# Kernel optimization log

Measured on AMD Instinct MI355X. Metric: run time of the kernel, lower is better.

Reference implementation:

```python
import jax, jax.numpy as jnp
import numpy as np

N = 2_000_000
FEAT = 128
S = 8192


def setup_inputs() -> dict:
    key = jax.random.key(0)
    k1, k2, k3, k4, k5 = jax.random.split(key, 5)
    x = jax.random.normal(k1, (N, FEAT), dtype=jnp.float32)
    subst_ids = jax.random.randint(k2, (N,), 0, S, dtype=jnp.int32)
    W1 = jax.random.normal(k3, (FEAT, 64), dtype=jnp.float32) * (1.0 / np.sqrt(FEAT))
    b1 = jax.random.normal(k4, (64,), dtype=jnp.float32) * 0.01
    w2 = jax.random.normal(k5, (64, 1), dtype=jnp.float32) * (1.0 / 8.0)
    return {"x": x, "subst_ids": subst_ids, "num_segments": S,
            "W1": W1, "b1": b1, "w2": w2}


def reference(x, subst_ids, num_segments, W1, b1, w2):
    # Segment mean over substructure ids (fused segment_sum + count).
    seg_sum = jax.ops.segment_sum(x, subst_ids, num_segments=num_segments)  # [S, F]
    counts = jax.ops.segment_sum(jnp.ones((x.shape[0],), x.dtype), subst_ids,
                                 num_segments=num_segments)                 # [S]
    means = seg_sum / jnp.maximum(counts, 1.0)[:, None]                     # [S, F]
    # Tiny attention MLP: Linear -> tanh -> Linear(no bias).
    scores = jnp.tanh(means @ W1 + b1) @ w2                                 # [S, 1]
    subst_attn = jax.nn.softmax(scores, axis=0)                             # [S, 1]
    # Scatter per-substructure attention back to each atom.
    atom_attn = subst_attn[subst_ids, 0]                                    # [N]
    return atom_attn[:, None]                                               # [N, 1]
```

## Files before the change

kernel.cpp:

```cpp
#include <hip/hip_runtime.h>
#include <math.h>

#define FEAT 128
#define SEG 8192
#define HID 64
#define CAP 512

typedef float f32x4 __attribute__((ext_vector_type(4)));

__global__ void scatter_kernel(const int* __restrict__ ids, int* __restrict__ cursor,
                               int* __restrict__ perm, int n) {
    const int tid = blockIdx.x * blockDim.x + threadIdx.x;
    const int stride = gridDim.x * blockDim.x;
    const int nv = n >> 2;
    for (int i = tid; i < nv; i += stride) {
        const int4 v = *reinterpret_cast<const int4*>(ids + i * 4);
        const int b = i * 4;
        int s0 = atomicAdd(&cursor[v.x], 1);
        int s1 = atomicAdd(&cursor[v.y], 1);
        int s2 = atomicAdd(&cursor[v.z], 1);
        int s3 = atomicAdd(&cursor[v.w], 1);
        if (s0 < CAP) perm[(v.x << 9) + s0] = b;
        if (s1 < CAP) perm[(v.y << 9) + s1] = b + 1;
        if (s2 < CAP) perm[(v.z << 9) + s2] = b + 2;
        if (s3 < CAP) perm[(v.w << 9) + s3] = b + 3;
    }
    for (int i = nv * 4 + tid; i < n; i += stride) {
        const int s = ids[i];
        const int sl = atomicAdd(&cursor[s], 1);
        if (sl < CAP) perm[(s << 9) + sl] = i;
    }
}

__global__ __launch_bounds__(256) void seg_reduce_mlp(
    const float* __restrict__ x, const int* __restrict__ perm, const int* __restrict__ cursor,
    const float* __restrict__ W1, const float* __restrict__ b1,
    const float* __restrict__ w2, float* __restrict__ scores) {
    const int s = blockIdx.x;
    const int cnt = min(cursor[s], CAP);
    const int t = threadIdx.x;
    const int grp = t >> 5;
    const int ln = t & 31;

    __shared__ int sperm[CAP];
    __shared__ float ssum[8][128];
    __shared__ float smean[128];

    for (int j = t; j < cnt; j += 256) sperm[j] = perm[(s << 9) + j];
    __syncthreads();

    f32x4 acc = (f32x4)(0.f);
    const int m = cnt;
    int r = grp;
    for (; r + 56 < m; r += 64) {
        const f32x4 v0 = __builtin_nontemporal_load(
            reinterpret_cast<const f32x4*>(x + (size_t)sperm[r] * FEAT + ln * 4));
        const f32x4 v1 = __builtin_nontemporal_load(
            reinterpret_cast<const f32x4*>(x + (size_t)sperm[r + 8] * FEAT + ln * 4));
        const f32x4 v2 = __builtin_nontemporal_load(
            reinterpret_cast<const f32x4*>(x + (size_t)sperm[r + 16] * FEAT + ln * 4));
        const f32x4 v3 = __builtin_nontemporal_load(
            reinterpret_cast<const f32x4*>(x + (size_t)sperm[r + 24] * FEAT + ln * 4));
        const f32x4 v4 = __builtin_nontemporal_load(
            reinterpret_cast<const f32x4*>(x + (size_t)sperm[r + 32] * FEAT + ln * 4));
        const f32x4 v5 = __builtin_nontemporal_load(
            reinterpret_cast<const f32x4*>(x + (size_t)sperm[r + 40] * FEAT + ln * 4));
        const f32x4 v6 = __builtin_nontemporal_load(
            reinterpret_cast<const f32x4*>(x + (size_t)sperm[r + 48] * FEAT + ln * 4));
        const f32x4 v7 = __builtin_nontemporal_load(
            reinterpret_cast<const f32x4*>(x + (size_t)sperm[r + 56] * FEAT + ln * 4));
        acc += ((v0 + v1) + (v2 + v3)) + ((v4 + v5) + (v6 + v7));
    }
    for (; r + 24 < m; r += 32) {
        const f32x4 v0 = __builtin_nontemporal_load(
            reinterpret_cast<const f32x4*>(x + (size_t)sperm[r] * FEAT + ln * 4));
        const f32x4 v1 = __builtin_nontemporal_load(
            reinterpret_cast<const f32x4*>(x + (size_t)sperm[r + 8] * FEAT + ln * 4));
        const f32x4 v2 = __builtin_nontemporal_load(
            reinterpret_cast<const f32x4*>(x + (size_t)sperm[r + 16] * FEAT + ln * 4));
        const f32x4 v3 = __builtin_nontemporal_load(
            reinterpret_cast<const f32x4*>(x + (size_t)sperm[r + 24] * FEAT + ln * 4));
        acc += (v0 + v1) + (v2 + v3);
    }
    for (; r < m; r += 8) {
        acc += __builtin_nontemporal_load(
            reinterpret_cast<const f32x4*>(x + (size_t)sperm[r] * FEAT + ln * 4));
    }

    *reinterpret_cast<f32x4*>(&ssum[grp][ln * 4]) = acc;
    __syncthreads();

    if (t < 128) {
        float tot = 0.f;
        #pragma unroll
        for (int g = 0; g < 8; ++g) tot += ssum[g][t];
        smean[t] = tot / fmaxf((float)cnt, 1.0f);
    }
    __syncthreads();

    if (t < 64) {
        float h = b1[t];
        #pragma unroll
        for (int ff = 0; ff < FEAT; ++ff) h = fmaf(smean[ff], W1[ff * HID + t], h);
        float v = tanhf(h) * w2[t];
        #pragma unroll
        for (int off = 32; off; off >>= 1) v += __shfl_down(v, off, 64);
        if (t == 0) scores[s] = v;
    }
}

__global__ void softmax8192(const float* __restrict__ scores, float* __restrict__ attn) {
    __shared__ float sval[SEG];
    __shared__ float red[16];
    __shared__ float red2[16];
    const int T = blockDim.x;
    const int t = threadIdx.x;
    const int wid = t >> 6, lane = t & 63;

    float m = -1e30f;
    for (int i = t; i < SEG; i += T) {
        const float v = scores[i];
        sval[i] = v;
        m = fmaxf(m, v);
    }
    #pragma unroll
    for (int off = 32; off; off >>= 1) m = fmaxf(m, __shfl_xor(m, off, 64));
    if (lane == 0) red[wid] = m;
    __syncthreads();
    if (t == 0) {
        float mm = red[0];
        for (int i = 1; i < 16; ++i) mm = fmaxf(mm, red[i]);
        red[0] = mm;
    }
    __syncthreads();
    m = red[0];

    float sum = 0.0f;
    for (int i = t; i < SEG; i += T) sum += expf(sval[i] - m);
    #pragma unroll
    for (int off = 32; off; off >>= 1) sum += __shfl_xor(sum, off, 64);
    if (lane == 0) red2[wid] = sum;
    __syncthreads();
    if (t == 0) {
        float ss = 0.0f;
        for (int i = 0; i < 16; ++i) ss += red2[i];
        red2[0] = ss;
    }
    __syncthreads();
    const float invZ = 1.0f / red2[0];
    for (int i = t; i < SEG; i += T) attn[i] = expf(sval[i] - m) * invZ;
}

__global__ void gather_attn(const int* __restrict__ ids, const float* __restrict__ attn,
                            float* __restrict__ out, int n) {
    const int i = blockIdx.x * blockDim.x + threadIdx.x;
    const int i4 = i * 4;
    if (i4 + 3 < n) {
        const int4 id4 = *reinterpret_cast<const int4*>(ids + i4);
        f32x4 o;
        o.x = attn[id4.x];
        o.y = attn[id4.y];
        o.z = attn[id4.z];
        o.w = attn[id4.w];
        __builtin_nontemporal_store(o, reinterpret_cast<f32x4*>(out + i4));
    } else {
        for (int k = i4; k < n; ++k) out[k] = attn[ids[k]];
    }
}

extern "C" void kernel_launch(void* const* d_in, const int* in_sizes, int n_in,
                              void* d_out, int out_size, void* d_ws, size_t ws_size,
                              hipStream_t stream) {
    const float* x   = (const float*)d_in[0];
    const int*   ids = (const int*)d_in[1];
    const float* W1  = (const float*)d_in[3];
    const float* b1  = (const float*)d_in[4];
    const float* w2  = (const float*)d_in[5];
    float* out = (float*)d_out;
    const int n = in_sizes[1];

    char* ws = (char*)d_ws;
    int*   cursor = (int*)ws;
    float* scores = (float*)(cursor + SEG);
    float* attn   = scores + SEG;
    int*   perm   = (int*)(attn + SEG);

    hipMemsetAsync(cursor, 0, SEG * sizeof(int), stream);

    scatter_kernel<<<2048, 256, 0, stream>>>(ids, cursor, perm, n);
    seg_reduce_mlp<<<SEG, 256, 0, stream>>>(x, perm, cursor, W1, b1, w2, scores);
    softmax8192<<<1, 1024, 0, stream>>>(scores, attn);

    const int nv = (n + 3) / 4;
    gather_attn<<<(nv + 255) / 256, 256, 0, stream>>>(ids, attn, out, n);
}
```

Before: 257.2 us.

## Fuse softmax into gather kernel and widen scatter loads to eight ids

Removes the single-block softmax kernel. Each of the ~1954 gather blocks now recomputes the 8192-entry softmax redundantly in shared memory and then gathers from LDS instead of global attn. The scatter kernel now handles eight ids per thread with nontemporal loads and a grid sized to the data, the perm staging uses 128-bit copies, and address math switches to 32-bit shifts. The fusion saves one launch and a serial single-block phase, but every gather block pays for 32K score reads and 8192 expf calls.

```diff
diff --git a/kernel.cpp b/kernel.cpp
--- a/kernel.cpp
+++ b/kernel.cpp
@@ -7,25 +7,38 @@
 #define CAP 512
 
 typedef float f32x4 __attribute__((ext_vector_type(4)));
+typedef int   i32x4 __attribute__((ext_vector_type(4)));
 
-__global__ void scatter_kernel(const int* __restrict__ ids, int* __restrict__ cursor,
-                               int* __restrict__ perm, int n) {
+__global__ __launch_bounds__(256) void scatter_kernel(
+    const int* __restrict__ ids, int* __restrict__ cursor,
+    int* __restrict__ perm, int n) {
     const int tid = blockIdx.x * blockDim.x + threadIdx.x;
     const int stride = gridDim.x * blockDim.x;
-    const int nv = n >> 2;
-    for (int i = tid; i < nv; i += stride) {
-        const int4 v = *reinterpret_cast<const int4*>(ids + i * 4);
-        const int b = i * 4;
-        int s0 = atomicAdd(&cursor[v.x], 1);
-        int s1 = atomicAdd(&cursor[v.y], 1);
-        int s2 = atomicAdd(&cursor[v.z], 1);
-        int s3 = atomicAdd(&cursor[v.w], 1);
-        if (s0 < CAP) perm[(v.x << 9) + s0] = b;
-        if (s1 < CAP) perm[(v.y << 9) + s1] = b + 1;
-        if (s2 < CAP) perm[(v.z << 9) + s2] = b + 2;
-        if (s3 < CAP) perm[(v.w << 9) + s3] = b + 3;
+    const int nv2 = n >> 3;
+    for (int i = tid; i < nv2; i += stride) {
+        const i32x4 a = __builtin_nontemporal_load(
+            reinterpret_cast<const i32x4*>(ids + i * 8));
+        const i32x4 b = __builtin_nontemporal_load(
+            reinterpret_cast<const i32x4*>(ids + i * 8 + 4));
+        const int base = i * 8;
+        const int s0 = atomicAdd(&cursor[a.x], 1);
+        const int s1 = atomicAdd(&cursor[a.y], 1);
+        const int s2 = atomicAdd(&cursor[a.z], 1);
+        const int s3 = atomicAdd(&cursor[a.w], 1);
+        const int s4 = atomicAdd(&cursor[b.x], 1);
+        const int s5 = atomicAdd(&cursor[b.y], 1);
+        const int s6 = atomicAdd(&cursor[b.z], 1);
+        const int s7 = atomicAdd(&cursor[b.w], 1);
+        if (s0 < CAP) perm[(a.x << 9) + s0] = base;
+        if (s1 < CAP) perm[(a.y << 9) + s1] = base + 1;
+        if (s2 < CAP) perm[(a.z << 9) + s2] = base + 2;
+        if (s3 < CAP) perm[(a.w << 9) + s3] = base + 3;
+        if (s4 < CAP) perm[(b.x << 9) + s4] = base + 4;
+        if (s5 < CAP) perm[(b.y << 9) + s5] = base + 5;
+        if (s6 < CAP) perm[(b.z << 9) + s6] = base + 6;
+        if (s7 < CAP) perm[(b.w << 9) + s7] = base + 7;
     }
-    for (int i = nv * 4 + tid; i < n; i += stride) {
+    for (int i = nv2 * 8 + tid; i < n; i += stride) {
         const int s = ids[i];
         const int sl = atomicAdd(&cursor[s], 1);
         if (sl < CAP) perm[(s << 9) + sl] = i;
@@ -40,13 +53,16 @@
     const int cnt = min(cursor[s], CAP);
     const int t = threadIdx.x;
     const int grp = t >> 5;
-    const int ln = t & 31;
+    const unsigned lnoff = (t & 31) << 2;
 
     __shared__ int sperm[CAP];
     __shared__ float ssum[8][128];
     __shared__ float smean[128];
 
-    for (int j = t; j < cnt; j += 256) sperm[j] = perm[(s << 9) + j];
+    const int nc4 = (cnt + 3) >> 2;
+    const i32x4* pb = reinterpret_cast<const i32x4*>(perm + (s << 9));
+    i32x4* sp4 = reinterpret_cast<i32x4*>(sperm);
+    for (int j = t; j < nc4; j += 256) sp4[j] = pb[j];
     __syncthreads();
 
     f32x4 acc = (f32x4)(0.f);
@@ -54,40 +70,40 @@
     int r = grp;
     for (; r + 56 < m; r += 64) {
         const f32x4 v0 = __builtin_nontemporal_load(
-            reinterpret_cast<const f32x4*>(x + (size_t)sperm[r] * FEAT + ln * 4));
+            reinterpret_cast<const f32x4*>(x + (((unsigned)sperm[r]      << 7) + lnoff)));
         const f32x4 v1 = __builtin_nontemporal_load(
-            reinterpret_cast<const f32x4*>(x + (size_t)sperm[r + 8] * FEAT + ln * 4));
+            reinterpret_cast<const f32x4*>(x + (((unsigned)sperm[r + 8]  << 7) + lnoff)));
         const f32x4 v2 = __builtin_nontemporal_load(
-            reinterpret_cast<const f32x4*>(x + (size_t)sperm[r + 16] * FEAT + ln * 4));
+            reinterpret_cast<const f32x4*>(x + (((unsigned)sperm[r + 16] << 7) + lnoff)));
         const f32x4 v3 = __builtin_nontemporal_load(
-            reinterpret_cast<const f32x4*>(x + (size_t)sperm[r + 24] * FEAT + ln * 4));
+            reinterpret_cast<const f32x4*>(x + (((unsigned)sperm[r + 24] << 7) + lnoff)));
         const f32x4 v4 = __builtin_nontemporal_load(
-            reinterpret_cast<const f32x4*>(x + (size_t)sperm[r + 32] * FEAT + ln * 4));
+            reinterpret_cast<const f32x4*>(x + (((unsigned)sperm[r + 32] << 7) + lnoff)));
         const f32x4 v5 = __builtin_nontemporal_load(
-            reinterpret_cast<const f32x4*>(x + (size_t)sperm[r + 40] * FEAT + ln * 4));
+            reinterpret_cast<const f32x4*>(x + (((unsigned)sperm[r + 40] << 7) + lnoff)));
         const f32x4 v6 = __builtin_nontemporal_load(
-            reinterpret_cast<const f32x4*>(x + (size_t)sperm[r + 48] * FEAT + ln * 4));
+            reinterpret_cast<const f32x4*>(x + (((unsigned)sperm[r + 48] << 7) + lnoff)));
         const f32x4 v7 = __builtin_nontemporal_load(
-            reinterpret_cast<const f32x4*>(x + (size_t)sperm[r + 56] * FEAT + ln * 4));
+            reinterpret_cast<const f32x4*>(x + (((unsigned)sperm[r + 56] << 7) + lnoff)));
         acc += ((v0 + v1) + (v2 + v3)) + ((v4 + v5) + (v6 + v7));
     }
     for (; r + 24 < m; r += 32) {
         const f32x4 v0 = __builtin_nontemporal_load(
-            reinterpret_cast<const f32x4*>(x + (size_t)sperm[r] * FEAT + ln * 4));
+            reinterpret_cast<const f32x4*>(x + (((unsigned)sperm[r]      << 7) + lnoff)));
         const f32x4 v1 = __builtin_nontemporal_load(
-            reinterpret_cast<const f32x4*>(x + (size_t)sperm[r + 8] * FEAT + ln * 4));
+            reinterpret_cast<const f32x4*>(x + (((unsigned)sperm[r + 8]  << 7) + lnoff)));
         const f32x4 v2 = __builtin_nontemporal_load(
-            reinterpret_cast<const f32x4*>(x + (size_t)sperm[r + 16] * FEAT + ln * 4));
+            reinterpret_cast<const f32x4*>(x + (((unsigned)sperm[r + 16] << 7) + lnoff)));
         const f32x4 v3 = __builtin_nontemporal_load(
-            reinterpret_cast<const f32x4*>(x + (size_t)sperm[r + 24] * FEAT + ln * 4));
+            reinterpret_cast<const f32x4*>(x + (((unsigned)sperm[r + 24] << 7) + lnoff)));
         acc += (v0 + v1) + (v2 + v3);
     }
     for (; r < m; r += 8) {
         acc += __builtin_nontemporal_load(
-            reinterpret_cast<const f32x4*>(x + (size_t)sperm[r] * FEAT + ln * 4));
+            reinterpret_cast<const f32x4*>(x + (((unsigned)sperm[r] << 7) + lnoff)));
     }
 
-    *reinterpret_cast<f32x4*>(&ssum[grp][ln * 4]) = acc;
+    *reinterpret_cast<f32x4*>(&ssum[grp][lnoff]) = acc;
     __syncthreads();
 
     if (t < 128) {
@@ -109,62 +125,48 @@
     }
 }
 
-__global__ void softmax8192(const float* __restrict__ scores, float* __restrict__ attn) {
-    __shared__ float sval[SEG];
-    __shared__ float red[16];
-    __shared__ float red2[16];
-    const int T = blockDim.x;
+__global__ __launch_bounds__(256) void softmax_gather(
+    const float* __restrict__ scores, const int* __restrict__ ids,
+    float* __restrict__ out, int n) {
+    __shared__ float sattn[SEG];
+    __shared__ float red[4];
     const int t = threadIdx.x;
     const int wid = t >> 6, lane = t & 63;
 
     float m = -1e30f;
-    for (int i = t; i < SEG; i += T) {
-        const float v = scores[i];
-        sval[i] = v;
-        m = fmaxf(m, v);
-    }
+    for (int i = t; i < SEG; i += 256) m = fmaxf(m, scores[i]);
     #pragma unroll
     for (int off = 32; off; off >>= 1) m = fmaxf(m, __shfl_xor(m, off, 64));
     if (lane == 0) red[wid] = m;
     __syncthreads();
-    if (t == 0) {
-        float mm = red[0];
-        for (int i = 1; i < 16; ++i) mm = fmaxf(mm, red[i]);
-        red[0] = mm;
+    m = fmaxf(fmaxf(red[0], red[1]), fmaxf(red[2], red[3]));
+
+    float sum = 0.f;
+    for (int i = t; i < SEG; i += 256) {
+        const float e = expf(scores[i] - m);
+        sattn[i] = e;
+        sum += e;
     }
-    __syncthreads();
-    m = red[0];
-
-    float sum = 0.0f;
-    for (int i = t; i < SEG; i += T) sum += expf(sval[i] - m);
     #pragma unroll
     for (int off = 32; off; off >>= 1) sum += __shfl_xor(sum, off, 64);
-    if (lane == 0) red2[wid] = sum;
     __syncthreads();
-    if (t == 0) {
-        float ss = 0.0f;
-        for (int i = 0; i < 16; ++i) ss += red2[i];
-        red2[0] = ss;
-    }
+    if (lane == 0) red[wid] = sum;
     __syncthreads();
-    const float invZ = 1.0f / red2[0];
-    for (int i = t; i < SEG; i += T) attn[i] = expf(sval[i] - m) * invZ;
-}
+    const float invZ = 1.0f / (((red[0] + red[1]) + (red[2] + red[3])));
 
-__global__ void gather_attn(const int* __restrict__ ids, const float* __restrict__ attn,
-                            float* __restrict__ out, int n) {
-    const int i = blockIdx.x * blockDim.x + threadIdx.x;
+    const int i = blockIdx.x * blockDim.x + t;
     const int i4 = i * 4;
     if (i4 + 3 < n) {
-        const int4 id4 = *reinterpret_cast<const int4*>(ids + i4);
+        const i32x4 id4 = __builtin_nontemporal_load(
+            reinterpret_cast<const i32x4*>(ids + i4));
         f32x4 o;
-        o.x = attn[id4.x];
-        o.y = attn[id4.y];
-        o.z = attn[id4.z];
-        o.w = attn[id4.w];
+        o.x = sattn[id4.x] * invZ;
+        o.y = sattn[id4.y] * invZ;
+        o.z = sattn[id4.z] * invZ;
+        o.w = sattn[id4.w] * invZ;
         __builtin_nontemporal_store(o, reinterpret_cast<f32x4*>(out + i4));
     } else {
-        for (int k = i4; k < n; ++k) out[k] = attn[ids[k]];
+        for (int k = i4; k < n; ++k) out[k] = sattn[ids[k]] * invZ;
     }
 }
 
@@ -182,15 +184,14 @@
     char* ws = (char*)d_ws;
     int*   cursor = (int*)ws;
     float* scores = (float*)(cursor + SEG);
-    float* attn   = scores + SEG;
-    int*   perm   = (int*)(attn + SEG);
+    int*   perm   = (int*)(scores + SEG);
 
     hipMemsetAsync(cursor, 0, SEG * sizeof(int), stream);
 
-    scatter_kernel<<<2048, 256, 0, stream>>>(ids, cursor, perm, n);
+    const int nv2 = n >> 3;
+    scatter_kernel<<<(nv2 + 255) / 256, 256, 0, stream>>>(ids, cursor, perm, n);
     seg_reduce_mlp<<<SEG, 256, 0, stream>>>(x, perm, cursor, W1, b1, w2, scores);
-    softmax8192<<<1, 1024, 0, stream>>>(scores, attn);
 
     const int nv = (n + 3) / 4;
-    gather_attn<<<(nv + 255) / 256, 256, 0, stream>>>(ids, attn, out, n);
+    softmax_gather<<<(nv + 255) / 256, 256, 0, stream>>>(scores, ids, out, n);
 }
```

Result: slower. 271.0 us (+5.4%).
